# Performance work log

Hardware: AMD Instinct MI355X
Metric: run time of the kernel (lower is better)

## Reference

```python
import jax, jax.numpy as jnp
import numpy as np

N = 100000      # num_edges in original graph = nodes here
E = 1600000     # edges of the line-graph
F_IN = 16       # num_edge_features
H, C = 2, 32    # heads, hidden_channels
HC = H * C
TD = 16         # time_embedding_dim
CD = 16         # condition_dim
NC = 2          # num_classes
MAX_TIME = 1000.0
THETA = 1.0


def _glorot(key, shape):
    fan_in = shape[0]
    return jax.random.normal(key, shape, dtype=jnp.float32) / np.sqrt(fan_in)


def setup_inputs() -> dict:
    key = jax.random.key(0)
    ks = jax.random.split(key, 32)
    inp = {
        "x": jax.random.normal(ks[0], (N, F_IN), dtype=jnp.float32),
        "edge_index": jax.random.randint(ks[1], (2, E), 0, N, dtype=jnp.int64),
        "t": jax.random.randint(ks[2], (1,), 0, 1000, dtype=jnp.int64),
        "condition": jax.random.normal(ks[3], (N, CD), dtype=jnp.float32),
        # GATv2 layer 0 (bias=True)
        "Wl0": _glorot(ks[4], (F_IN, HC)), "bl0": jnp.zeros((HC,), jnp.float32),
        "Wr0": _glorot(ks[5], (F_IN, HC)), "br0": jnp.zeros((HC,), jnp.float32),
        "att0": _glorot(ks[6], (H, C)), "bias0": jnp.zeros((HC,), jnp.float32),
        "Wres0": _glorot(ks[7], (F_IN, HC)), "bres0": jnp.zeros((HC,), jnp.float32),
        # GATv2 layer 1 (bias=False)
        "Wl1": _glorot(ks[8], (HC, HC)),
        "Wr1": _glorot(ks[9], (HC, HC)),
        "att1": _glorot(ks[10], (H, C)),
        "Wres1": _glorot(ks[11], (HC, HC)), "bres1": jnp.zeros((HC,), jnp.float32),
        # time MLP
        "Wt0": _glorot(ks[12], (TD, TD)), "bt0": jnp.zeros((TD,), jnp.float32),
        "Wt1": _glorot(ks[13], (TD, TD)), "bt1": jnp.zeros((TD,), jnp.float32),
        # decoder heads
        "Wfd": _glorot(ks[14], (HC + CD + TD, C)), "bfd": jnp.zeros((C,), jnp.float32),
        "Wcls": _glorot(ks[15], (C, NC)), "bcls": jnp.zeros((NC,), jnp.float32),
    }
    return inp


def _segment_softmax(logits, seg, num_seg):
    # logits: [E, H], softmax over edges sharing the same destination node
    m = jax.ops.segment_max(logits, seg, num_segments=num_seg)
    ex = jnp.exp(logits - m[seg])
    s = jax.ops.segment_sum(ex, seg, num_segments=num_seg)
    return ex / (s[seg] + 1e-16)


def _gatv2(x, src, dst, Wl, bl, Wr, br, att, bias):
    # PyG GATv2Conv with add_self_loops (self loops appended by caller)
    xl = x @ Wl
    xr = x @ Wr
    if bl is not None:
        xl = xl + bl
        xr = xr + br
    xl = xl.reshape(-1, H, C)
    xr = xr.reshape(-1, H, C)
    e = jax.nn.leaky_relu(xl[src] + xr[dst], negative_slope=0.2)  # [E, H, C]
    logits = jnp.einsum('ehc,hc->eh', e, att)                     # [E, H]
    alpha = _segment_softmax(logits, dst, N)                      # [E, H]
    msg = xl[src] * alpha[:, :, None]                             # [E, H, C]
    out = jax.ops.segment_sum(msg, dst, num_segments=N)           # [N, H, C]
    out = out.reshape(N, HC)
    if bias is not None:
        out = out + bias
    return out


def _time_embedding(t):
    tf = t.astype(jnp.float32) * (1000.0 / MAX_TIME)
    half = TD // 2
    freqs = jnp.exp(jnp.arange(half, dtype=jnp.float32) * -(jnp.log(10000.0) / (half - 1)))
    ang = tf[:, None] * freqs[None, :]
    return jnp.concatenate([jnp.sin(ang), jnp.cos(ang)], axis=1)  # [1, TD]


def reference(x, edge_index, t, condition,
              Wl0, bl0, Wr0, br0, att0, bias0, Wres0, bres0,
              Wl1, Wr1, att1, Wres1, bres1,
              Wt0, bt0, Wt1, bt1, Wfd, bfd, Wcls, bcls):
    loops = jnp.arange(N, dtype=edge_index.dtype)
    src = jnp.concatenate([edge_index[0], loops])
    dst = jnp.concatenate([edge_index[1], loops])

    # layer 0
    res = jax.nn.relu(x @ Wres0 + bres0)
    h = jax.nn.relu(_gatv2(x, src, dst, Wl0, bl0, Wr0, br0, att0, bias0))
    h = THETA * h + res
    # layer 1 (bias=False)
    res = jax.nn.relu(h @ Wres1 + bres1)
    h2 = jax.nn.relu(_gatv2(h, src, dst, Wl1, None, Wr1, None, att1, None))
    h = THETA * h2 + res

    # mode == 'future'
    t_emb = _time_embedding(t)
    t_emb = jax.nn.silu(t_emb @ Wt0 + bt0)
    t_emb = jax.nn.silu(t_emb @ Wt1 + bt1)
    t_rep = jnp.tile(t_emb, (N, 1))                                # [N, TD]
    h = jnp.concatenate([h, t_rep, condition], axis=1)             # [N, HC+TD+CD]
    logits = h @ Wfd + bfd
    logits = logits @ Wcls + bcls
    return logits[None]                                            # [1, N, NC]
```

## Files before the change

### kernel.cpp

```cpp
#include <hip/hip_runtime.h>
#include <hip/hip_bf16.h>
#include <hip/hip_fp16.h>
#include <math.h>


#define BLK 256
#define BDST 32
#define CDST 256
#define CHUNK 4096
#define FCAP 768
#define NBC_MAX 512

typedef _Float16 half4v __attribute__((ext_vector_type(4)));
typedef _Float16 half2v __attribute__((ext_vector_type(2)));

#if __has_builtin(__builtin_amdgcn_fdot2)
#define FDOT2(a, b, c) __builtin_amdgcn_fdot2((a), (b), (c), false)
#else
__device__ __forceinline__ float fdot2_fallback(half2v a, half2v b, float c) {
    return c + (float)a.x * (float)b.x + (float)a.y * (float)b.y;
}
#define FDOT2(a, b, c) fdot2_fallback((a), (b), (c))
#endif

__device__ __forceinline__ float leaky02(float x) { return x >= 0.f ? x : 0.2f * x; }
__device__ __forceinline__ float relu(float x) { return x > 0.f ? x : 0.f; }

__global__ void k_tiny(const int* __restrict__ t,
                       const float* __restrict__ Wt0, const float* __restrict__ bt0,
                       const float* __restrict__ Wt1, const float* __restrict__ bt1,
                       const float* __restrict__ Wfd, const float* __restrict__ bfd,
                       const float* __restrict__ Wcls, const float* __restrict__ bcls,
                       float* __restrict__ wcomb,
                       float* __restrict__ bfinal)
{
    __shared__ float temb[16];
    int tid = threadIdx.x;
    if (tid == 0) {
        float tf = (float)t[0];
        float e0[16], v1[16];
        const float cexp = -logf(10000.f) / 7.f;
        for (int j = 0; j < 8; ++j) {
            float ang = tf * expf((float)j * cexp);
            e0[j] = sinf(ang);
            e0[8 + j] = cosf(ang);
        }
        for (int i = 0; i < 16; ++i) {
            float a = bt0[i];
            for (int j = 0; j < 16; ++j) a += e0[j] * Wt0[j * 16 + i];
            v1[i] = a / (1.f + expf(-a));
        }
        for (int i = 0; i < 16; ++i) {
            float a = bt1[i];
            for (int j = 0; j < 16; ++j) a += v1[j] * Wt1[j * 16 + i];
            temb[i] = a / (1.f + expf(-a));
        }
    }
    __syncthreads();
    if (tid < 192) {
        int i = tid >> 1, k = tid & 1;
        float a = 0.f;
        for (int j = 0; j < 32; ++j) a += Wfd[i * 32 + j] * Wcls[j * 2 + k];
        wcomb[tid] = a;
    }
    __syncthreads();
    if (tid < 2) {
        float a = bcls[tid];
        for (int j = 0; j < 32; ++j) a += bfd[j] * Wcls[j * 2 + tid];
        for (int d = 0; d < 16; ++d) a += temb[d] * wcomb[(64 + d) * 2 + tid];
        bfinal[tid] = a;
    }
}

__global__ void k_zeroc(int* __restrict__ ccnt, int NBC)
{
    int gid = blockIdx.x * BLK + threadIdx.x;
    if (gid < NBC) ccnt[gid] = 0;
}

__global__ void k_histc(const int* __restrict__ ei, int E, int NBC,
                        int* __restrict__ ccnt)
{
    __shared__ int h[NBC_MAX];
    int tid = threadIdx.x;
    for (int i = tid; i < NBC; i += BLK) h[i] = 0;
    __syncthreads();
    int e0 = blockIdx.x * CHUNK;
    #pragma unroll
    for (int k = 0; k < CHUNK / BLK; ++k) {
        int e = e0 + tid + k * BLK;
        if (e < E) atomicAdd(&h[ei[E + e] >> 8], 1);
    }
    __syncthreads();
    for (int i = tid; i < NBC; i += BLK) {
        int v = h[i];
        if (v) atomicAdd(&ccnt[i], v);
    }
}

__global__ void k_scan(const int* __restrict__ ccnt, int NBC, int E,
                       int* __restrict__ cbase, int* __restrict__ ccur)
{
    if (threadIdx.x == 0) {
        int acc = 0;
        for (int i = 0; i < NBC; ++i) {
            cbase[i] = acc;
            acc += ccnt[i];
        }
        cbase[NBC] = acc;
    }
    __syncthreads();
    for (int i = threadIdx.x; i < NBC; i += BLK) ccur[i] = cbase[i];
}

__global__ void k_part(const int* __restrict__ ei, int E, int NBC,
                       int* __restrict__ ccur, int* __restrict__ part)
{
    __shared__ int h[NBC_MAX];
    __shared__ int gb[NBC_MAX];
    int tid = threadIdx.x;
    int e0 = blockIdx.x * CHUNK;
    for (int i = tid; i < NBC; i += BLK) h[i] = 0;
    __syncthreads();
    int sv[CHUNK / BLK], dv[CHUNK / BLK];
    #pragma unroll
    for (int k = 0; k < CHUNK / BLK; ++k) {
        int e = e0 + tid + k * BLK;
        if (e < E) {
            sv[k] = ei[e];
            dv[k] = ei[E + e];
            atomicAdd(&h[dv[k] >> 8], 1);
        } else dv[k] = -1;
    }
    __syncthreads();
    for (int i = tid; i < NBC; i += BLK) {
        int v = h[i];
        gb[i] = v ? atomicAdd(&ccur[i], v) : 0;
    }
    __syncthreads();
    for (int i = tid; i < NBC; i += BLK) h[i] = gb[i];
    __syncthreads();
    #pragma unroll
    for (int k = 0; k < CHUNK / BLK; ++k) {
        if (dv[k] >= 0) {
            int p = atomicAdd(&h[dv[k] >> 8], 1);
            part[p] = (sv[k] << 8) | (dv[k] & 255);
        }
    }
}

__global__ void k_refine(const int* __restrict__ cbase, const int* __restrict__ part,
                         int NBF, int* __restrict__ fbeg, int* __restrict__ fend,
                         int* __restrict__ srcs)
{
    __shared__ int fcnt[8];
    __shared__ int fcur[8];
    int b = blockIdx.x, tid = threadIdx.x;
    int beg = cbase[b], end = cbase[b + 1];
    if (tid < 8) fcnt[tid] = 0;
    __syncthreads();
    for (int k = beg + tid; k < end; k += BLK)
        atomicAdd(&fcnt[(part[k] >> 5) & 7], 1);
    __syncthreads();
    if (tid == 0) {
        int acc = beg;
        #pragma unroll
        for (int f = 0; f < 8; ++f) {
            int fb = b * 8 + f;
            fcur[f] = acc;
            if (fb < NBF) { fbeg[fb] = acc; acc += fcnt[f]; fend[fb] = acc; }
        }
    }
    __syncthreads();
    for (int k = beg + tid; k < end; k += BLK) {
        int tg = part[k];
        int p = atomicAdd(&fcur[(tg >> 5) & 7], 1);
        srcs[p] = ((tg >> 8) << 5) | (tg & 31);
    }
}

__global__ void k_pre0f(const float* __restrict__ x,
                        const float* __restrict__ Wl, const float* __restrict__ bl,
                        const float* __restrict__ Wr, const float* __restrict__ br,
                        const float* __restrict__ Wres, const float* __restrict__ bres,
                        _Float16* __restrict__ xlh, _Float16* __restrict__ xr16,
                        _Float16* __restrict__ res16, int N)
{
    int wid = (int)(((long long)blockIdx.x * BLK + threadIdx.x) >> 6);
    int lane = threadIdx.x & 63;
    int g = lane >> 4, q = lane & 15;
    int n = wid * 4 + g;
    bool valid = n < N;
    int nn = valid ? n : N - 1;
    float xv = x[(size_t)nn * 16 + q];
    int c0 = q * 4;
    float4 accl = *(const float4*)(bl + c0);
    float4 accr = *(const float4*)(br + c0);
    float4 accs = *(const float4*)(bres + c0);
    #pragma unroll
    for (int k = 0; k < 16; ++k) {
        float xk = __shfl(xv, (g << 4) | k, 64);
        float4 wl = *(const float4*)(Wl + k * 64 + c0);
        float4 wr = *(const float4*)(Wr + k * 64 + c0);
        float4 wsv = *(const float4*)(Wres + k * 64 + c0);
        accl.x = fmaf(xk, wl.x, accl.x);
        accl.y = fmaf(xk, wl.y, accl.y);
        accl.z = fmaf(xk, wl.z, accl.z);
        accl.w = fmaf(xk, wl.w, accl.w);
        accr.x = fmaf(xk, wr.x, accr.x);
        accr.y = fmaf(xk, wr.y, accr.y);
        accr.z = fmaf(xk, wr.z, accr.z);
        accr.w = fmaf(xk, wr.w, accr.w);
        accs.x = fmaf(xk, wsv.x, accs.x);
        accs.y = fmaf(xk, wsv.y, accs.y);
        accs.z = fmaf(xk, wsv.z, accs.z);
        accs.w = fmaf(xk, wsv.w, accs.w);
    }
    if (valid) {
        size_t base = (size_t)n * 64 + c0;
        half4v hl, hr, hs;
        hl.x = (_Float16)accl.x; hl.y = (_Float16)accl.y;
        hl.z = (_Float16)accl.z; hl.w = (_Float16)accl.w;
        hr.x = (_Float16)accr.x; hr.y = (_Float16)accr.y;
        hr.z = (_Float16)accr.z; hr.w = (_Float16)accr.w;
        hs.x = (_Float16)relu(accs.x); hs.y = (_Float16)relu(accs.y);
        hs.z = (_Float16)relu(accs.z); hs.w = (_Float16)relu(accs.w);
        *(half4v*)(xlh + base) = hl;
        *(half4v*)(xr16 + base) = hr;
        *(half4v*)(res16 + base) = hs;
    }
}

__global__ void k_pre1w(const _Float16* __restrict__ h16,
                        const float* __restrict__ Wl, const float* __restrict__ Wr,
                        const float* __restrict__ Wres, const float* __restrict__ bres,
                        _Float16* __restrict__ xlh, _Float16* __restrict__ xr16,
                        _Float16* __restrict__ res16, int N)
{
    __shared__ half4v wl4[16][64];
    __shared__ half4v wr4[16][64];
    __shared__ half4v ws4[16][64];
    __shared__ half4v h4[32][16];
    int tid = threadIdx.x;
    int nb = blockIdx.x * 32;

    for (int idx = tid; idx < 3 * 1024; idx += BLK) {
        int m = idx >> 10, rem = idx & 1023;
        int k4 = rem >> 6, c = rem & 63;
        const float* W = (m == 0) ? Wl : (m == 1) ? Wr : Wres;
        half4v v;
        v.x = (_Float16)W[(4 * k4 + 0) * 64 + c];
        v.y = (_Float16)W[(4 * k4 + 1) * 64 + c];
        v.z = (_Float16)W[(4 * k4 + 2) * 64 + c];
        v.w = (_Float16)W[(4 * k4 + 3) * 64 + c];
        (m == 0 ? wl4 : m == 1 ? wr4 : ws4)[k4][c] = v;
    }
    for (int idx = tid; idx < 512; idx += BLK) {
        int i = idx >> 4, k4 = idx & 15;
        int n = nb + i; if (n >= N) n = N - 1;
        h4[i][k4] = *(const half4v*)(h16 + (size_t)n * 64 + k4 * 4);
    }
    __syncthreads();

    int c = tid & 63, w = tid >> 6;
    float al[8], ar[8], as[8];
    float vbs = bres[c];
    #pragma unroll
    for (int i = 0; i < 8; ++i) { al[i] = 0.f; ar[i] = 0.f; as[i] = vbs; }

    #pragma unroll 4
    for (int k4 = 0; k4 < 16; ++k4) {
        half4v wl = wl4[k4][c];
        half4v wr = wr4[k4][c];
        half4v wsv = ws4[k4][c];
        half2v wll = { wl.x, wl.y },  wlh = { wl.z, wl.w };
        half2v wrl = { wr.x, wr.y },  wrh = { wr.z, wr.w };
        half2v wsl = { wsv.x, wsv.y }, wsh = { wsv.z, wsv.w };
        #pragma unroll
        for (int i = 0; i < 8; ++i) {
            half4v hv = h4[w * 8 + i][k4];
            half2v hl = { hv.x, hv.y }, hh = { hv.z, hv.w };
            al[i] = FDOT2(hl, wll, al[i]);
            al[i] = FDOT2(hh, wlh, al[i]);
            ar[i] = FDOT2(hl, wrl, ar[i]);
            ar[i] = FDOT2(hh, wrh, ar[i]);
            as[i] = FDOT2(hl, wsl, as[i]);
            as[i] = FDOT2(hh, wsh, as[i]);
        }
    }
    #pragma unroll
    for (int i = 0; i < 8; ++i) {
        int n = nb + w * 8 + i;
        if (n < N) {
            xlh[(size_t)n * 64 + c]   = (_Float16)al[i];
            xr16[(size_t)n * 64 + c]  = (_Float16)ar[i];
            res16[(size_t)n * 64 + c] = (_Float16)relu(as[i]);
        }
    }
}

template <bool DEC>
__global__ void k_gat3(const int* __restrict__ fbeg, const int* __restrict__ fend,
                       const int* __restrict__ srcs,
                       const _Float16* __restrict__ xlh, const _Float16* __restrict__ xr16,
                       const float* __restrict__ att, const float* __restrict__ bias,
                       const _Float16* __restrict__ res16,
                       _Float16* __restrict__ hout16,
                       const float* __restrict__ cond, const float* __restrict__ wcomb,
                       const float* __restrict__ bfinal, float* __restrict__ out,
                       int N)
{
    __shared__ int lh[BDST];
    __shared__ int rp[BDST + 1];
    __shared__ int cc[BDST];
    __shared__ int tags[FCAP];

    int b = blockIdx.x;
    int tid = threadIdx.x;
    int beg = fbeg[b];
    int nE = fend[b] - beg; if (nE > FCAP) nE = FCAP;

    if (tid < BDST) lh[tid] = 0;
    __syncthreads();
    for (int k = tid; k < nE; k += BLK) atomicAdd(&lh[srcs[beg + k] & 31], 1);
    __syncthreads();
    if (tid == 0) {
        int acc = 0;
        rp[0] = 0;
        #pragma unroll
        for (int i = 0; i < BDST; ++i) { acc += lh[i]; rp[i + 1] = acc; }
    }
    __syncthreads();
    if (tid < BDST) cc[tid] = rp[tid];
    __syncthreads();
    for (int k = tid; k < nE; k += BLK) {
        int tg = srcs[beg + k];
        int r = atomicAdd(&cc[tg & 31], 1);
        tags[r] = tg >> 5;
    }
    __syncthreads();

    int lane = tid & 63, w = tid >> 6;
    int g = lane >> 4, q = lane & 15;
    int c0 = q * 4;
    float4 a4 = *(const float4*)(att + c0);

    #pragma unroll
    for (int rep = 0; rep < 2; ++rep) {
        int dlow = w * 8 + rep * 4 + g;
        int node = b * BDST + dlow;
        bool nvalid = node < N;
        int n = nvalid ? node : 0;

        half4v xrh = *(const half4v*)(xr16 + (size_t)n * 64 + c0);
        float xrx = (float)xrh.x, xry = (float)xrh.y, xrz = (float)xrh.z, xrw = (float)xrh.w;

        half4v hs = *(const half4v*)(xlh + (size_t)n * 64 + c0);
        float s0 = (float)hs.x, s1 = (float)hs.y, s2 = (float)hs.z, s3 = (float)hs.w;
        float lv = leaky02(s0 + xrx) * a4.x + leaky02(s1 + xry) * a4.y
                 + leaky02(s2 + xrz) * a4.z + leaky02(s3 + xrw) * a4.w;
        lv += __shfl_xor(lv, 1, 8);
        lv += __shfl_xor(lv, 2, 8);
        lv += __shfl_xor(lv, 4, 8);

        float m = lv, den = 1.f;
        float ac0 = s0, ac1 = s1, ac2 = s2, ac3 = s3;

        int deg = nvalid ? (rp[dlow + 1] - rp[dlow]) : 0;
        int base = nvalid ? rp[dlow] : 0;

        int t1 = max(deg, __shfl_xor(deg, 16, 64));
        int wavemax = max(t1, __shfl_xor(t1, 32, 64));

        int i1 = (0 < deg) ? tags[base] : n;
        int i2 = (1 < deg) ? tags[base + 1] : n;
        half4v p1 = *(const half4v*)(xlh + (size_t)i1 * 64 + c0);
        half4v p2 = *(const half4v*)(xlh + (size_t)i2 * 64 + c0);

        for (int j = 0; j < wavemax; j += 2) {
            bool a1 = j < deg, a2 = j + 1 < deg;
            half4v h1 = p1, h2 = p2;
            int n1 = (j + 2 < deg) ? tags[base + j + 2] : n;
            int n2 = (j + 3 < deg) ? tags[base + j + 3] : n;
            p1 = *(const half4v*)(xlh + (size_t)n1 * 64 + c0);
            p2 = *(const half4v*)(xlh + (size_t)n2 * 64 + c0);

            float x10 = (float)h1.x, x11 = (float)h1.y, x12 = (float)h1.z, x13 = (float)h1.w;
            float x20 = (float)h2.x, x21 = (float)h2.y, x22 = (float)h2.z, x23 = (float)h2.w;
            float e1 = leaky02(x10 + xrx) * a4.x + leaky02(x11 + xry) * a4.y
                     + leaky02(x12 + xrz) * a4.z + leaky02(x13 + xrw) * a4.w;
            float e2 = leaky02(x20 + xrx) * a4.x + leaky02(x21 + xry) * a4.y
                     + leaky02(x22 + xrz) * a4.z + leaky02(x23 + xrw) * a4.w;
            e1 += __shfl_xor(e1, 1, 8);
            e2 += __shfl_xor(e2, 1, 8);
            e1 += __shfl_xor(e1, 2, 8);
            e2 += __shfl_xor(e2, 2, 8);
            e1 += __shfl_xor(e1, 4, 8);
            e2 += __shfl_xor(e2, 4, 8);
            if (!a1) e1 = -1e30f;
            if (!a2) e2 = -1e30f;

            float mn = fmaxf(m, fmaxf(e1, e2));
            float sc  = __expf(m - mn);
            float ex1 = __expf(e1 - mn);
            float ex2 = __expf(e2 - mn);
            den = den * sc + ex1 + ex2;
            ac0 = ac0 * sc + ex1 * x10 + ex2 * x20;
            ac1 = ac1 * sc + ex1 * x11 + ex2 * x21;
            ac2 = ac2 * sc + ex1 * x12 + ex2 * x22;
            ac3 = ac3 * sc + ex1 * x13 + ex2 * x23;
            m = mn;
        }

        float inv = 1.f / den;
        half4v rh = *(const half4v*)(res16 + (size_t)n * 64 + c0);
        float h0, h1, h2, h3;
        if (bias) {
            const float4 b4 = *(const float4*)(bias + c0);
            h0 = relu(ac0 * inv + b4.x) + (float)rh.x;
            h1 = relu(ac1 * inv + b4.y) + (float)rh.y;
            h2 = relu(ac2 * inv + b4.z) + (float)rh.z;
            h3 = relu(ac3 * inv + b4.w) + (float)rh.w;
        } else {
            h0 = relu(ac0 * inv) + (float)rh.x;
            h1 = relu(ac1 * inv) + (float)rh.y;
            h2 = relu(ac2 * inv) + (float)rh.z;
            h3 = relu(ac3 * inv) + (float)rh.w;
        }

        if (!DEC) {
            if (nvalid) {
                half4v o;
                o.x = (_Float16)h0; o.y = (_Float16)h1;
                o.z = (_Float16)h2; o.w = (_Float16)h3;
                *(half4v*)(hout16 + (size_t)n * 64 + c0) = o;
            }
        } else {
            float p0 = h0 * wcomb[(c0 + 0) * 2] + h1 * wcomb[(c0 + 1) * 2]
                     + h2 * wcomb[(c0 + 2) * 2] + h3 * wcomb[(c0 + 3) * 2];
            float p1d = h0 * wcomb[(c0 + 0) * 2 + 1] + h1 * wcomb[(c0 + 1) * 2 + 1]
                      + h2 * wcomb[(c0 + 2) * 2 + 1] + h3 * wcomb[(c0 + 3) * 2 + 1];
            if (q < 4) {
                float4 c4 = *(const float4*)(cond + (size_t)n * 16 + q * 4);
                int d0 = 80 + q * 4;
                p0 += c4.x * wcomb[(d0 + 0) * 2] + c4.y * wcomb[(d0 + 1) * 2]
                    + c4.z * wcomb[(d0 + 2) * 2] + c4.w * wcomb[(d0 + 3) * 2];
                p1d += c4.x * wcomb[(d0 + 0) * 2 + 1] + c4.y * wcomb[(d0 + 1) * 2 + 1]
                     + c4.z * wcomb[(d0 + 2) * 2 + 1] + c4.w * wcomb[(d0 + 3) * 2 + 1];
            }
            #pragma unroll
            for (int off = 1; off < 16; off <<= 1) {
                p0 += __shfl_xor(p0, off, 16);
                p1d += __shfl_xor(p1d, off, 16);
            }
            if (q == 0 && nvalid) {
                out[(size_t)n * 2] = p0 + bfinal[0];
                out[(size_t)n * 2 + 1] = p1d + bfinal[1];
            }
        }
    }
}

static inline int gblk(long long threads) { return (int)((threads + BLK - 1) / BLK); }

extern "C" void kernel_launch(void* const* d_in, const int* in_sizes, int n_in,
                              void* d_out, int out_size, void* d_ws, size_t ws_size,
                              hipStream_t stream) {
    const float* x     = (const float*)d_in[0];
    const int*   ei    = (const int*)d_in[1];
    const int*   t     = (const int*)d_in[2];
    const float* cond  = (const float*)d_in[3];
    const float* Wl0   = (const float*)d_in[4];
    const float* bl0   = (const float*)d_in[5];
    const float* Wr0   = (const float*)d_in[6];
    const float* br0   = (const float*)d_in[7];
    const float* att0  = (const float*)d_in[8];
    const float* bias0 = (const float*)d_in[9];
    const float* Wres0 = (const float*)d_in[10];
    const float* bres0 = (const float*)d_in[11];
    const float* Wl1   = (const float*)d_in[12];
    const float* Wr1   = (const float*)d_in[13];
    const float* att1  = (const float*)d_in[14];
    const float* Wres1 = (const float*)d_in[15];
    const float* bres1 = (const float*)d_in[16];
    const float* Wt0   = (const float*)d_in[17];
    const float* bt0   = (const float*)d_in[18];
    const float* Wt1   = (const float*)d_in[19];
    const float* bt1   = (const float*)d_in[20];
    const float* Wfd   = (const float*)d_in[21];
    const float* bfd   = (const float*)d_in[22];
    const float* Wcls  = (const float*)d_in[23];
    const float* bcls  = (const float*)d_in[24];
    float* out = (float*)d_out;

    const int N   = in_sizes[0] / 16;
    const int E   = in_sizes[1] / 2;
    const int NBC = (N + CDST - 1) / CDST;
    const int NBF = (N + BDST - 1) / BDST;

    float* ws = (float*)d_ws;
    size_t o = 0;
    _Float16* hbuf16 = (_Float16*)(ws + o); o += (size_t)N * 32;
    _Float16* xlh    = (_Float16*)(ws + o); o += (size_t)N * 32;
    _Float16* xr16   = (_Float16*)(ws + o); o += (size_t)N * 32;
    _Float16* res16  = (_Float16*)(ws + o); o += (size_t)N * 32;
    float* wcomb = ws + o; o += 192;
    float* bfin  = ws + o; o += 2;
    int* iws     = (int*)(ws + o);
    size_t io = 0;
    int* ccnt  = iws + io; io += NBC_MAX;
    int* cbase = iws + io; io += NBC_MAX + 1;
    int* ccur  = iws + io; io += NBC_MAX;
    int* fbeg  = iws + io; io += NBF;
    int* fend  = iws + io; io += NBF;
    int* part  = iws + io; io += E;
    int* srcs  = iws + io; io += E;

    const int partBlocks = (E + CHUNK - 1) / CHUNK;

    k_tiny<<<1, BLK, 0, stream>>>(t, Wt0, bt0, Wt1, bt1, Wfd, bfd, Wcls, bcls, wcomb, bfin);

    k_zeroc<<<gblk(NBC), BLK, 0, stream>>>(ccnt, NBC);
    k_histc<<<partBlocks, BLK, 0, stream>>>(ei, E, NBC, ccnt);
    k_scan<<<1, BLK, 0, stream>>>(ccnt, NBC, E, cbase, ccur);
    k_part<<<partBlocks, BLK, 0, stream>>>(ei, E, NBC, ccur, part);
    k_refine<<<NBC, BLK, 0, stream>>>(cbase, part, NBF, fbeg, fend, srcs);

    k_pre0f<<<gblk((long long)((N + 3) / 4) * 64), BLK, 0, stream>>>(
        x, Wl0, bl0, Wr0, br0, Wres0, bres0, xlh, xr16, res16, N);
    k_gat3<false><<<NBF, BLK, 0, stream>>>(fbeg, fend, srcs, xlh, xr16, att0, bias0, res16,
                                           hbuf16, nullptr, nullptr, nullptr, nullptr, N);

    k_pre1w<<<(N + 31) / 32, BLK, 0, stream>>>(hbuf16, Wl1, Wr1, Wres1, bres1, xlh, xr16, res16, N);
    k_gat3<true><<<NBF, BLK, 0, stream>>>(fbeg, fend, srcs, xlh, xr16, att1, nullptr, res16,
                                          nullptr, cond, wcomb, bfin, out, N);
}
```

Baseline: 293.6 us.

## Sort destinations by degree, unroll edge loop by four, use packed fp16 scoring

Each block now ranks its 32 destination nodes by in-degree and assigns them to wave slots in sorted order, so nodes of similar degree share a wave and fewer lanes idle while waiting on the longest node. The online-softmax edge loop is unrolled from two to four gathered neighbours per iteration, with four prefetched rows to raise memory-level parallelism. The attention logit is computed with packed fp16 adds, max-based leaky ReLU and fdot2 instead of fp32 scalar math. The fp16 logit arithmetic loses some precision, and the wider unroll raises register pressure.

```diff
diff --git a/kernel.cpp b/kernel.cpp
--- a/kernel.cpp
+++ b/kernel.cpp
@@ -25,6 +25,15 @@
 
 __device__ __forceinline__ float leaky02(float x) { return x >= 0.f ? x : 0.2f * x; }
 __device__ __forceinline__ float relu(float x) { return x > 0.f ? x : 0.f; }
+
+__device__ __forceinline__ float edot(half4v h, half2v xlo, half2v xhi,
+                                      half2v alo, half2v ahi, half2v c02) {
+    half2v lo = half2v{h.x, h.y} + xlo;
+    half2v hi = half2v{h.z, h.w} + xhi;
+    lo = __builtin_elementwise_max(lo, lo * c02);
+    hi = __builtin_elementwise_max(hi, hi * c02);
+    return FDOT2(lo, alo, FDOT2(hi, ahi, 0.f));
+}
 
 __global__ void k_tiny(const int* __restrict__ t,
                        const float* __restrict__ Wt0, const float* __restrict__ bt0,
@@ -313,6 +322,7 @@
     __shared__ int lh[BDST];
     __shared__ int rp[BDST + 1];
     __shared__ int cc[BDST];
+    __shared__ int sidx[BDST];
     __shared__ int tags[FCAP];
 
     int b = blockIdx.x;
@@ -338,33 +348,45 @@
         int r = atomicAdd(&cc[tg & 31], 1);
         tags[r] = tg >> 5;
     }
+    if (tid < BDST) {
+        int di = rp[tid + 1] - rp[tid];
+        int r = 0;
+        #pragma unroll
+        for (int j = 0; j < BDST; ++j) {
+            int dj = rp[j + 1] - rp[j];
+            r += (dj > di) || (dj == di && j < tid);
+        }
+        sidx[r] = tid;
+    }
     __syncthreads();
 
     int lane = tid & 63, w = tid >> 6;
     int g = lane >> 4, q = lane & 15;
     int c0 = q * 4;
-    float4 a4 = *(const float4*)(att + c0);
+    float4 a4f = *(const float4*)(att + c0);
+    const half2v c02 = { (_Float16)0.2f, (_Float16)0.2f };
+    half2v alo = { (_Float16)a4f.x, (_Float16)a4f.y };
+    half2v ahi = { (_Float16)a4f.z, (_Float16)a4f.w };
 
     #pragma unroll
     for (int rep = 0; rep < 2; ++rep) {
-        int dlow = w * 8 + rep * 4 + g;
+        int dlow = sidx[w * 8 + rep * 4 + g];
         int node = b * BDST + dlow;
         bool nvalid = node < N;
         int n = nvalid ? node : 0;
 
         half4v xrh = *(const half4v*)(xr16 + (size_t)n * 64 + c0);
-        float xrx = (float)xrh.x, xry = (float)xrh.y, xrz = (float)xrh.z, xrw = (float)xrh.w;
-
-        half4v hs = *(const half4v*)(xlh + (size_t)n * 64 + c0);
-        float s0 = (float)hs.x, s1 = (float)hs.y, s2 = (float)hs.z, s3 = (float)hs.w;
-        float lv = leaky02(s0 + xrx) * a4.x + leaky02(s1 + xry) * a4.y
-                 + leaky02(s2 + xrz) * a4.z + leaky02(s3 + xrw) * a4.w;
+        half2v xlo = { xrh.x, xrh.y }, xhi = { xrh.z, xrh.w };
+
+        half4v hsv = *(const half4v*)(xlh + (size_t)n * 64 + c0);
+        float lv = edot(hsv, xlo, xhi, alo, ahi, c02);
         lv += __shfl_xor(lv, 1, 8);
         lv += __shfl_xor(lv, 2, 8);
         lv += __shfl_xor(lv, 4, 8);
 
         float m = lv, den = 1.f;
-        float ac0 = s0, ac1 = s1, ac2 = s2, ac3 = s3;
+        float ac0 = (float)hsv.x, ac1 = (float)hsv.y;
+        float ac2 = (float)hsv.z, ac3 = (float)hsv.w;
 
         int deg = nvalid ? (rp[dlow + 1] - rp[dlow]) : 0;
         int base = nvalid ? rp[dlow] : 0;
@@ -372,43 +394,57 @@
         int t1 = max(deg, __shfl_xor(deg, 16, 64));
         int wavemax = max(t1, __shfl_xor(t1, 32, 64));
 
-        int i1 = (0 < deg) ? tags[base] : n;
+        int i1 = (0 < deg) ? tags[base + 0] : n;
         int i2 = (1 < deg) ? tags[base + 1] : n;
+        int i3 = (2 < deg) ? tags[base + 2] : n;
+        int i4 = (3 < deg) ? tags[base + 3] : n;
         half4v p1 = *(const half4v*)(xlh + (size_t)i1 * 64 + c0);
         half4v p2 = *(const half4v*)(xlh + (size_t)i2 * 64 + c0);
-
-        for (int j = 0; j < wavemax; j += 2) {
-            bool a1 = j < deg, a2 = j + 1 < deg;
-            half4v h1 = p1, h2 = p2;
-            int n1 = (j + 2 < deg) ? tags[base + j + 2] : n;
-            int n2 = (j + 3 < deg) ? tags[base + j + 3] : n;
+        half4v p3 = *(const half4v*)(xlh + (size_t)i3 * 64 + c0);
+        half4v p4 = *(const half4v*)(xlh + (size_t)i4 * 64 + c0);
+
+        for (int j = 0; j < wavemax; j += 4) {
+            bool a1 = j < deg, a2 = j + 1 < deg, a3 = j + 2 < deg, a4b = j + 3 < deg;
+            half4v h1 = p1, h2 = p2, h3 = p3, h4 = p4;
+            int n1 = (j + 4 < deg) ? tags[base + j + 4] : n;
+            int n2 = (j + 5 < deg) ? tags[base + j + 5] : n;
+            int n3 = (j + 6 < deg) ? tags[base + j + 6] : n;
+            int n4 = (j + 7 < deg) ? tags[base + j + 7] : n;
             p1 = *(const half4v*)(xlh + (size_t)n1 * 64 + c0);
             p2 = *(const half4v*)(xlh + (size_t)n2 * 64 + c0);
-
-            float x10 = (float)h1.x, x11 = (float)h1.y, x12 = (float)h1.z, x13 = (float)h1.w;
-            float x20 = (float)h2.x, x21 = (float)h2.y, x22 = (float)h2.z, x23 = (float)h2.w;
-            float e1 = leaky02(x10 + xrx) * a4.x + leaky02(x11 + xry) * a4.y
-                     + leaky02(x12 + xrz) * a4.z + leaky02(x13 + xrw) * a4.w;
-            float e2 = leaky02(x20 + xrx) * a4.x + leaky02(x21 + xry) * a4.y
-                     + leaky02(x22 + xrz) * a4.z + leaky02(x23 + xrw) * a4.w;
-            e1 += __shfl_xor(e1, 1, 8);
-            e2 += __shfl_xor(e2, 1, 8);
-            e1 += __shfl_xor(e1, 2, 8);
-            e2 += __shfl_xor(e2, 2, 8);
-            e1 += __shfl_xor(e1, 4, 8);
-            e2 += __shfl_xor(e2, 4, 8);
+            p3 = *(const half4v*)(xlh + (size_t)n3 * 64 + c0);
+            p4 = *(const half4v*)(xlh + (size_t)n4 * 64 + c0);
+
+            float e1 = edot(h1, xlo, xhi, alo, ahi, c02);
+            float e2 = edot(h2, xlo, xhi, alo, ahi, c02);
+            float e3 = edot(h3, xlo, xhi, alo, ahi, c02);
+            float e4 = edot(h4, xlo, xhi, alo, ahi, c02);
+            e1 += __shfl_xor(e1, 1, 8); e2 += __shfl_xor(e2, 1, 8);
+            e3 += __shfl_xor(e3, 1, 8); e4 += __shfl_xor(e4, 1, 8);
+            e1 += __shfl_xor(e1, 2, 8); e2 += __shfl_xor(e2, 2, 8);
+            e3 += __shfl_xor(e3, 2, 8); e4 += __shfl_xor(e4, 2, 8);
+            e1 += __shfl_xor(e1, 4, 8); e2 += __shfl_xor(e2, 4, 8);
+            e3 += __shfl_xor(e3, 4, 8); e4 += __shfl_xor(e4, 4, 8);
             if (!a1) e1 = -1e30f;
             if (!a2) e2 = -1e30f;
-
-            float mn = fmaxf(m, fmaxf(e1, e2));
+            if (!a3) e3 = -1e30f;
+            if (!a4b) e4 = -1e30f;
+
+            float mn = fmaxf(fmaxf(m, fmaxf(e1, e2)), fmaxf(e3, e4));
             float sc  = __expf(m - mn);
             float ex1 = __expf(e1 - mn);
             float ex2 = __expf(e2 - mn);
-            den = den * sc + ex1 + ex2;
-            ac0 = ac0 * sc + ex1 * x10 + ex2 * x20;
-            ac1 = ac1 * sc + ex1 * x11 + ex2 * x21;
-            ac2 = ac2 * sc + ex1 * x12 + ex2 * x22;
-            ac3 = ac3 * sc + ex1 * x13 + ex2 * x23;
+            float ex3 = __expf(e3 - mn);
+            float ex4 = __expf(e4 - mn);
+            den = den * sc + ((ex1 + ex2) + (ex3 + ex4));
+            ac0 = fmaf(ex4, (float)h4.x, fmaf(ex3, (float)h3.x,
+                  fmaf(ex2, (float)h2.x, fmaf(ex1, (float)h1.x, ac0 * sc))));
+            ac1 = fmaf(ex4, (float)h4.y, fmaf(ex3, (float)h3.y,
+                  fmaf(ex2, (float)h2.y, fmaf(ex1, (float)h1.y, ac1 * sc))));
+            ac2 = fmaf(ex4, (float)h4.z, fmaf(ex3, (float)h3.z,
+                  fmaf(ex2, (float)h2.z, fmaf(ex1, (float)h1.z, ac2 * sc))));
+            ac3 = fmaf(ex4, (float)h4.w, fmaf(ex3, (float)h3.w,
+                  fmaf(ex2, (float)h2.w, fmaf(ex1, (float)h1.w, ac3 * sc))));
             m = mn;
         }
 
```

Result: faster. 274.4 us (-6.5%).
